# Kernel tuning notes

Hardware: AMD Instinct MI355X
Metric: run time of the kernel (lower is better)

The kernel has to match this reference:

```python
import jax, jax.numpy as jnp
import numpy as np


def _ens_linear(x, W, b):
    # x: [B,T,Din], W: [E,Din,Dout], b: [E,Dout] -> [E,B,T,Dout]
    return jnp.einsum('btd,edh->ebth', x, W) + b[:, None, None, :]


def _gilr_scan(v, f):
    # h_t = f_t * h_{t-1} + (1 - f_t) * v_t, h_0 = 0 (tie-input-gate linear recurrence)
    def comb(c1, c2):
        a1, b1 = c1
        a2, b2 = c2
        return a2 * a1, a2 * b1 + b2
    _, h = jax.lax.associative_scan(comb, (f, (1.0 - f) * v), axis=1)
    return h


def setup_inputs() -> dict:
    key = jax.random.key(0)
    ks = jax.random.split(key, 7)
    B, T, Din, D = 8, 4096, 512, 512
    x = jax.random.normal(ks[0], (B, T, Din), dtype=jnp.float32)
    s_in = 1.0 / np.sqrt(Din)
    s = 1.0 / np.sqrt(D)
    W_in = jax.random.uniform(ks[1], (2, Din, D), jnp.float32, -s_in, s_in)
    b_in = jax.random.uniform(ks[2], (2, D), jnp.float32, -s_in, s_in)
    W_mid = jax.random.uniform(ks[3], (4, D, D), jnp.float32, -s, s)
    b_mid = jax.random.uniform(ks[4], (4, D), jnp.float32, -s, s)
    W_out = jax.random.uniform(ks[5], (D, D), jnp.float32, -s, s)
    b_out = jax.random.uniform(ks[6], (D,), jnp.float32, -s, s)
    return {"x": x, "W_in": W_in, "b_in": b_in, "W_mid": W_mid,
            "b_mid": b_mid, "W_out": W_out, "b_out": b_out}


def reference(x, W_in, b_in, W_mid, b_mid, W_out, b_out):
    # in_proj (ensemble of 2): u[0] -> v, u[1] -> f
    u = _ens_linear(x, W_in, b_in)
    v = jnp.tanh(u[0])
    f = jax.nn.sigmoid(u[1])
    # first gated linear recurrence (hidden_pre starts at zeros)
    v = _gilr_scan(v, f)
    hidden_pre = v[:, -1:, :]
    # middle_proj (ensemble of 4): f, i, o, z
    u = _ens_linear(v, W_mid, b_mid)
    f2 = jax.nn.sigmoid(u[0])
    i = jax.nn.sigmoid(u[1])
    o = jax.nn.sigmoid(u[2])
    z = jnp.tanh(u[3])
    # second gated linear recurrence (hidden_middle starts at zeros)
    out = _gilr_scan(i * z, f2)
    hidden_middle = out[:, -1:, :]
    out = out * o
    out = out @ W_out + b_out
    hidden = jnp.concatenate((hidden_pre, hidden_middle), axis=-1)
    hidden = jnp.transpose(hidden, (1, 0, 2))  # [1, B, 2D]
    return out, hidden
```

## Files before the change

### kernel.cpp

```cpp
#include <hip/hip_runtime.h>

typedef short short8 __attribute__((ext_vector_type(8)));
typedef float float4v __attribute__((ext_vector_type(4)));
typedef unsigned short u16;
typedef unsigned int u32;

#define T_LEN 4096
#define DDIM 512
#define BATCH 8
#define MROWS 32768
#define CH 32
#define NC 128

__device__ __forceinline__ u16 f2b(float x) {
    unsigned u = __float_as_uint(x);
    unsigned r = (u + 0x7FFFu + ((u >> 16) & 1u)) >> 16;
    return (u16)r;
}
__device__ __forceinline__ float b2f(u16 h) {
    return __uint_as_float((u32)h << 16);
}
__device__ __forceinline__ float sigm(float x) {
    return __builtin_amdgcn_rcpf(1.f + __builtin_amdgcn_exp2f(-1.44269504f * x));
}
__device__ __forceinline__ float tanh_fast(float x) {
    return 1.f - 2.f * __builtin_amdgcn_rcpf(1.f + __builtin_amdgcn_exp2f(2.88539008f * x));
}

__device__ __forceinline__ void gl2lds16(const u16* g, u16* l) {
    __builtin_amdgcn_global_load_lds(
        (const __attribute__((address_space(1))) void*)g,
        (__attribute__((address_space(3))) void*)l, 16, 0, 0);
}

__global__ __launch_bounds__(256) void cvt_x(const float* __restrict__ x,
                                             u16* __restrict__ xb, size_t n) {
    size_t i = ((size_t)blockIdx.x * 256 + threadIdx.x) * 4;
    if (i < n) {
        float4v v = *(const float4v*)&x[i];
        ushort4 p;
        p.x = f2b(v[0]); p.y = f2b(v[1]); p.z = f2b(v[2]); p.w = f2b(v[3]);
        *(ushort4*)&xb[i] = p;
    }
}

__global__ __launch_bounds__(256) void cvt_wt(const float* __restrict__ W,
                                              u16* __restrict__ Wt, int N) {
    int idx = blockIdx.x * 256 + threadIdx.x;
    if (idx >= N * 512) return;
    int j = idx >> 9;
    int k = idx & 511;
    int e = j >> 9, h = j & 511;
    Wt[(size_t)j * 512 + k] = f2b(W[((size_t)e * 512 + k) * 512 + h]);
}

template <int MODE>
__global__ __launch_bounds__(512, 4) void gemm_act(
    const u16* __restrict__ A, const u16* __restrict__ Bt,
    const float* __restrict__ bias, void* __restrict__ o0v,
    void* __restrict__ o1v, void* __restrict__ o2v, void* __restrict__ o3v) {
    constexpr int K = 512;
    constexpr int BK = 32;
    constexpr int NKT = K / BK;
    constexpr int LBA = 256 * 32;
    constexpr int LBB = 128 * 32;
    constexpr int GX = (MODE == 1) ? 8 : (MODE == 2) ? 16 : 4;
    constexpr int NWG = 128 * GX;
    __shared__ u16 lsA[3][LBA];
    __shared__ u16 lsB[3][LBB];
    const int tid = threadIdx.x;
    const int lane = tid & 63;
    const int wid = tid >> 6;
    const int wr = wid >> 1;
    const int wc = wid & 1;
    const int l0 = lane & 15, lh = lane >> 4;

    const int h = blockIdx.x;
    const int l = (h & 7) * (NWG / 8) + (h >> 3);
    const int bn0 = (l & (GX - 1)) * 128;
    const int bm0 = (l / GX) * 256;

    float4v acc[4][4];
#pragma unroll
    for (int m = 0; m < 4; ++m)
#pragma unroll
        for (int n = 0; n < 4; ++n) acc[m][n] = (float4v){0.f, 0.f, 0.f, 0.f};

    int growA[2], gchA[2], growB, gchB;
#pragma unroll
    for (int i = 0; i < 2; ++i) {
        int flat = i * 512 + tid;
        growA[i] = flat >> 2;
        gchA[i] = (((flat & 3) ^ ((growA[i] >> 1) & 3))) * 8;
    }
    growB = tid >> 2;
    gchB = (((tid & 3) ^ ((growB >> 1) & 3))) * 8;

#define STAGE(buf, kt)                                                        \
    {                                                                         \
        const int k0 = (kt) * BK;                                             \
        _Pragma("unroll") for (int i = 0; i < 2; ++i)                         \
            gl2lds16(&A[(size_t)(bm0 + growA[i]) * K + k0 + gchA[i]],         \
                     &lsA[buf][(i * 512 + tid) * 8]);                         \
        gl2lds16(&Bt[(size_t)(bn0 + growB) * K + k0 + gchB],                  \
                 &lsB[buf][tid * 8]);                                         \
    }

    STAGE(0, 0);
    STAGE(1, 1);

    for (int kt = 0; kt < NKT; ++kt) {
        const int cur = kt % 3;
        if (kt + 1 < NKT)
            asm volatile("s_waitcnt vmcnt(3)" ::: "memory");
        else
            asm volatile("s_waitcnt vmcnt(0)" ::: "memory");
        __builtin_amdgcn_s_barrier();
        __builtin_amdgcn_sched_barrier(0);
        if (kt + 2 < NKT) STAGE((kt + 2) % 3, kt + 2);
        short8 af[4], bf[4];
#pragma unroll
        for (int m = 0; m < 4; ++m) {
            int r = wr * 64 + m * 16 + l0;
            af[m] = *(const short8*)&lsA[cur][r * 32 + ((lh ^ ((r >> 1) & 3)) * 8)];
        }
#pragma unroll
        for (int n = 0; n < 4; ++n) {
            int r = wc * 64 + n * 16 + l0;
            bf[n] = *(const short8*)&lsB[cur][r * 32 + ((lh ^ ((r >> 1) & 3)) * 8)];
        }
        asm volatile("s_waitcnt lgkmcnt(0)" ::: "memory");
        __builtin_amdgcn_sched_barrier(0);
        __builtin_amdgcn_s_setprio(1);
#pragma unroll
        for (int m = 0; m < 4; ++m)
#pragma unroll
            for (int n = 0; n < 4; ++n)
                acc[m][n] = __builtin_amdgcn_mfma_f32_16x16x32_bf16(
                    af[m], bf[n], acc[m][n], 0, 0, 0);
        __builtin_amdgcn_s_setprio(0);
    }
#undef STAGE

#pragma unroll
    for (int m = 0; m < 4; ++m) {
#pragma unroll
        for (int n = 0; n < 4; ++n) {
            int col = bn0 + wc * 64 + n * 16 + l0;
            float bv = bias[col];
#pragma unroll
            for (int r = 0; r < 4; ++r) {
                int rw = bm0 + wr * 64 + m * 16 + lh * 4 + r;
                float u = acc[m][n][r] + bv;
                size_t oidx = (size_t)rw * 512 + (col & 511);
                if (MODE == 1) {
                    if (col < 512)
                        ((u16*)o0v)[oidx] = f2b(tanh_fast(u));
                    else
                        ((u16*)o1v)[oidx] = f2b(sigm(u));
                } else if (MODE == 2) {
                    int e = col >> 9;
                    if (e == 0)
                        ((u16*)o0v)[oidx] = f2b(sigm(u));
                    else if (e == 1)
                        ((u16*)o1v)[oidx] = f2b(sigm(u));
                    else if (e == 2)
                        ((u16*)o2v)[oidx] = f2b(sigm(u));
                    else
                        ((u16*)o3v)[oidx] = f2b(tanh_fast(u));
                } else {
                    ((float*)o0v)[oidx] = u;
                }
            }
        }
    }
}

template <int S>
__global__ __launch_bounds__(128) void scan_p1(const u16* __restrict__ f,
                                               const u16* __restrict__ v,
                                               const u16* __restrict__ z,
                                               float* __restrict__ cA,
                                               float* __restrict__ cB) {
    int d0 = threadIdx.x * 4;
    int c = blockIdx.x & (NC - 1);
    int b = blockIdx.x >> 7;
    size_t base = ((size_t)b * T_LEN + c * CH) * DDIM + d0;
    float Aa[4] = {1.f, 1.f, 1.f, 1.f}, Bb[4] = {0.f, 0.f, 0.f, 0.f};
    for (int t = 0; t < CH; ++t) {
        ushort4 fq = *(const ushort4*)&f[base];
        ushort4 vq = *(const ushort4*)&v[base];
        float ff[4] = {b2f(fq.x), b2f(fq.y), b2f(fq.z), b2f(fq.w)};
        float gg[4] = {b2f(vq.x), b2f(vq.y), b2f(vq.z), b2f(vq.w)};
        if (S == 2) {
            ushort4 zq = *(const ushort4*)&z[base];
            gg[0] *= b2f(zq.x); gg[1] *= b2f(zq.y);
            gg[2] *= b2f(zq.z); gg[3] *= b2f(zq.w);
        }
#pragma unroll
        for (int j = 0; j < 4; ++j) {
            float g = (1.f - ff[j]) * gg[j];
            Bb[j] = ff[j] * Bb[j] + g;
            Aa[j] *= ff[j];
        }
        base += DDIM;
    }
    size_t ci = (size_t)c * 4096 + b * DDIM + d0;
#pragma unroll
    for (int j = 0; j < 4; ++j) {
        cA[ci + j] = Aa[j];
        cB[ci + j] = Bb[j];
    }
}

__global__ __launch_bounds__(256) void scan_p2(float* __restrict__ cA,
                                               const float* __restrict__ cB) {
    int ln = blockIdx.x * 256 + threadIdx.x;
    float h = 0.f;
    for (int c = 0; c < NC; ++c) {
        size_t ix = (size_t)c * 4096 + ln;
        float a = cA[ix], bb = cB[ix];
        cA[ix] = h;
        h = a * h + bb;
    }
}

template <int S>
__global__ __launch_bounds__(128) void scan_p3(
    const u16* __restrict__ f, const u16* __restrict__ v,
    const u16* __restrict__ z, const u16* __restrict__ o,
    const float* __restrict__ cA, u16* __restrict__ hb,
    float* __restrict__ hid) {
    int d0 = threadIdx.x * 4;
    int c = blockIdx.x & (NC - 1);
    int b = blockIdx.x >> 7;
    size_t base = ((size_t)b * T_LEN + c * CH) * DDIM + d0;
    size_t ci = (size_t)c * 4096 + b * DDIM + d0;
    float h[4] = {cA[ci], cA[ci + 1], cA[ci + 2], cA[ci + 3]};
    for (int t = 0; t < CH; ++t) {
        ushort4 fq = *(const ushort4*)&f[base];
        ushort4 vq = *(const ushort4*)&v[base];
        float ff[4] = {b2f(fq.x), b2f(fq.y), b2f(fq.z), b2f(fq.w)};
        float gg[4] = {b2f(vq.x), b2f(vq.y), b2f(vq.z), b2f(vq.w)};
        if (S == 2) {
            ushort4 zq = *(const ushort4*)&z[base];
            gg[0] *= b2f(zq.x); gg[1] *= b2f(zq.y);
            gg[2] *= b2f(zq.z); gg[3] *= b2f(zq.w);
        }
        float w[4];
#pragma unroll
        for (int j = 0; j < 4; ++j) {
            float g = (1.f - ff[j]) * gg[j];
            h[j] = ff[j] * h[j] + g;
            w[j] = h[j];
        }
        if (S == 2) {
            ushort4 oq = *(const ushort4*)&o[base];
            w[0] *= b2f(oq.x); w[1] *= b2f(oq.y);
            w[2] *= b2f(oq.z); w[3] *= b2f(oq.w);
        }
        ushort4 p;
        p.x = f2b(w[0]); p.y = f2b(w[1]); p.z = f2b(w[2]); p.w = f2b(w[3]);
        *(ushort4*)&hb[base] = p;
        base += DDIM;
    }
    if (c == NC - 1) {
#pragma unroll
        for (int j = 0; j < 4; ++j)
            hid[b * 1024 + (S == 1 ? 0 : 512) + d0 + j] = h[j];
    }
}

extern "C" void kernel_launch(void* const* d_in, const int* in_sizes, int n_in,
                              void* d_out, int out_size, void* d_ws,
                              size_t ws_size, hipStream_t stream) {
    const float* x = (const float*)d_in[0];
    const float* W_in = (const float*)d_in[1];
    const float* b_in = (const float*)d_in[2];
    const float* W_mid = (const float*)d_in[3];
    const float* b_mid = (const float*)d_in[4];
    const float* W_out = (const float*)d_in[5];
    const float* b_out = (const float*)d_in[6];
    float* out = (float*)d_out;
    char* ws = (char*)d_ws;

    const size_t MB = 1u << 20;
    const size_t MD = (size_t)MROWS * DDIM;

    u16* wt_in = (u16*)(ws);
    u16* wt_mid = (u16*)(ws + 1 * MB);
    u16* wt_out = (u16*)(ws + 3 * MB);
    u16* hb = (u16*)(ws + 4 * MB);
    u16* S0 = (u16*)(ws + 36 * MB);
    u16* S1 = (u16*)(ws + 68 * MB);
    u16* S2 = (u16*)(ws + 100 * MB);
    u16* S3 = (u16*)(ws + 132 * MB);
    float* cA = (float*)(ws + 164 * MB);
    float* cB = (float*)(ws + 166 * MB);
    float* hid = out + MD;

    cvt_x<<<(int)(MD / 4 / 256), 256, 0, stream>>>(x, hb, MD);
    cvt_wt<<<(1024 * 512) / 256, 256, 0, stream>>>(W_in, wt_in, 1024);
    cvt_wt<<<(2048 * 512) / 256, 256, 0, stream>>>(W_mid, wt_mid, 2048);
    cvt_wt<<<(512 * 512) / 256, 256, 0, stream>>>(W_out, wt_out, 512);

    gemm_act<1><<<1024, 512, 0, stream>>>(hb, wt_in, b_in, S0, S1, nullptr,
                                          nullptr);
    scan_p1<1><<<1024, 128, 0, stream>>>(S1, S0, nullptr, cA, cB);
    scan_p2<<<16, 256, 0, stream>>>(cA, cB);
    scan_p3<1><<<1024, 128, 0, stream>>>(S1, S0, nullptr, nullptr, cA, hb, hid);

    gemm_act<2><<<2048, 512, 0, stream>>>(hb, wt_mid, b_mid, S0, S1, S2, S3);
    scan_p1<2><<<1024, 128, 0, stream>>>(S0, S1, S3, cA, cB);
    scan_p2<<<16, 256, 0, stream>>>(cA, cB);
    scan_p3<2><<<1024, 128, 0, stream>>>(S0, S1, S3, S2, cA, hb, hid);

    gemm_act<3><<<512, 512, 0, stream>>>(hb, wt_out, b_out, out, nullptr,
                                         nullptr, nullptr);
}
```

Baseline: 292.7 us.

## Interleave gate weight columns so GEMM epilogue precomputes gated scan input

Weight columns are reordered during conversion so each wave's accumulator tile holds the matching f/v (or f/i/o/z) gates for the same hidden index. The GEMM epilogue then computes (1-f)*tanh(v) and (1-f)*i*z directly and writes only f, g and o. The scan kernels read two streams instead of three or four. This removes one bf16 intermediate buffer per stage and its write/read traffic, at the cost of a more complex epilogue with strided column writes of 16-element groups.

New measurement: 259.7 us. 11.3% less time.

```diff
diff --git a/kernel.cpp b/kernel.cpp
--- a/kernel.cpp
+++ b/kernel.cpp
@@ -44,21 +44,25 @@
     }
 }
 
+template <int MODE>
 __global__ __launch_bounds__(256) void cvt_wt(const float* __restrict__ W,
                                               u16* __restrict__ Wt, int N) {
     int idx = blockIdx.x * 256 + threadIdx.x;
     if (idx >= N * 512) return;
     int j = idx >> 9;
     int k = idx & 511;
-    int e = j >> 9, h = j & 511;
-    Wt[(size_t)j * 512 + k] = f2b(W[((size_t)e * 512 + k) * 512 + h]);
+    int gate, d;
+    if (MODE == 1) { gate = (j >> 4) & 1; d = (j >> 5) * 16 + (j & 15); }
+    else if (MODE == 2) { gate = (j >> 4) & 3; d = (j >> 6) * 16 + (j & 15); }
+    else { gate = 0; d = j; }
+    Wt[(size_t)j * 512 + k] = f2b(W[((size_t)gate * 512 + k) * 512 + d]);
 }
 
 template <int MODE>
 __global__ __launch_bounds__(512, 4) void gemm_act(
     const u16* __restrict__ A, const u16* __restrict__ Bt,
     const float* __restrict__ bias, void* __restrict__ o0v,
-    void* __restrict__ o1v, void* __restrict__ o2v, void* __restrict__ o3v) {
+    void* __restrict__ o1v, void* __restrict__ o2v) {
     constexpr int K = 512;
     constexpr int BK = 32;
     constexpr int NKT = K / BK;
@@ -142,44 +146,64 @@
     }
 #undef STAGE
 
-#pragma unroll
-    for (int m = 0; m < 4; ++m) {
-#pragma unroll
-        for (int n = 0; n < 4; ++n) {
-            int col = bn0 + wc * 64 + n * 16 + l0;
-            float bv = bias[col];
+    if (MODE == 3) {
+#pragma unroll
+        for (int m = 0; m < 4; ++m) {
+#pragma unroll
+            for (int n = 0; n < 4; ++n) {
+                int col = bn0 + wc * 64 + n * 16 + l0;
+                float bv = bias[col];
+#pragma unroll
+                for (int r = 0; r < 4; ++r) {
+                    int rw = bm0 + wr * 64 + m * 16 + lh * 4 + r;
+                    ((float*)o0v)[(size_t)rw * 512 + col] = acc[m][n][r] + bv;
+                }
+            }
+        }
+    } else if (MODE == 1) {
+        const int base5 = (bn0 + wc * 64) >> 5;
+#pragma unroll
+        for (int p = 0; p < 2; ++p) {
+            const int d = (base5 + p) * 16 + l0;
+            const float bvv = bias[d], bvf = bias[512 + d];
+#pragma unroll
+            for (int m = 0; m < 4; ++m) {
+#pragma unroll
+                for (int r = 0; r < 4; ++r) {
+                    int rw = bm0 + wr * 64 + m * 16 + lh * 4 + r;
+                    float f1 = sigm(acc[m][2 * p + 1][r] + bvf);
+                    float g = (1.f - f1) * tanh_fast(acc[m][2 * p][r] + bvv);
+                    size_t oidx = (size_t)rw * 512 + d;
+                    ((u16*)o0v)[oidx] = f2b(f1);
+                    ((u16*)o1v)[oidx] = f2b(g);
+                }
+            }
+        }
+    } else {
+        const int d = ((bn0 + wc * 64) >> 6) * 16 + l0;
+        const float bv0 = bias[d], bv1 = bias[512 + d];
+        const float bv2 = bias[1024 + d], bv3 = bias[1536 + d];
+#pragma unroll
+        for (int m = 0; m < 4; ++m) {
 #pragma unroll
             for (int r = 0; r < 4; ++r) {
                 int rw = bm0 + wr * 64 + m * 16 + lh * 4 + r;
-                float u = acc[m][n][r] + bv;
-                size_t oidx = (size_t)rw * 512 + (col & 511);
-                if (MODE == 1) {
-                    if (col < 512)
-                        ((u16*)o0v)[oidx] = f2b(tanh_fast(u));
-                    else
-                        ((u16*)o1v)[oidx] = f2b(sigm(u));
-                } else if (MODE == 2) {
-                    int e = col >> 9;
-                    if (e == 0)
-                        ((u16*)o0v)[oidx] = f2b(sigm(u));
-                    else if (e == 1)
-                        ((u16*)o1v)[oidx] = f2b(sigm(u));
-                    else if (e == 2)
-                        ((u16*)o2v)[oidx] = f2b(sigm(u));
-                    else
-                        ((u16*)o3v)[oidx] = f2b(tanh_fast(u));
-                } else {
-                    ((float*)o0v)[oidx] = u;
-                }
+                float f2 = sigm(acc[m][0][r] + bv0);
+                float ii = sigm(acc[m][1][r] + bv1);
+                float oo = sigm(acc[m][2][r] + bv2);
+                float zz = tanh_fast(acc[m][3][r] + bv3);
+                float g = (1.f - f2) * ii * zz;
+                size_t oidx = (size_t)rw * 512 + d;
+                ((u16*)o0v)[oidx] = f2b(f2);
+                ((u16*)o1v)[oidx] = f2b(g);
+                ((u16*)o2v)[oidx] = f2b(oo);
             }
         }
     }
 }
 
-template <int S>
 __global__ __launch_bounds__(128) void scan_p1(const u16* __restrict__ f,
-                                               const u16* __restrict__ v,
-                                               const u16* __restrict__ z,
+                                               const u16* __restrict__ g,
                                                float* __restrict__ cA,
                                                float* __restrict__ cB) {
     int d0 = threadIdx.x * 4;
@@ -189,18 +213,12 @@
     float Aa[4] = {1.f, 1.f, 1.f, 1.f}, Bb[4] = {0.f, 0.f, 0.f, 0.f};
     for (int t = 0; t < CH; ++t) {
         ushort4 fq = *(const ushort4*)&f[base];
-        ushort4 vq = *(const ushort4*)&v[base];
+        ushort4 gq = *(const ushort4*)&g[base];
         float ff[4] = {b2f(fq.x), b2f(fq.y), b2f(fq.z), b2f(fq.w)};
-        float gg[4] = {b2f(vq.x), b2f(vq.y), b2f(vq.z), b2f(vq.w)};
-        if (S == 2) {
-            ushort4 zq = *(const ushort4*)&z[base];
-            gg[0] *= b2f(zq.x); gg[1] *= b2f(zq.y);
-            gg[2] *= b2f(zq.z); gg[3] *= b2f(zq.w);
-        }
+        float gg[4] = {b2f(gq.x), b2f(gq.y), b2f(gq.z), b2f(gq.w)};
 #pragma unroll
         for (int j = 0; j < 4; ++j) {
-            float g = (1.f - ff[j]) * gg[j];
-            Bb[j] = ff[j] * Bb[j] + g;
+            Bb[j] = ff[j] * Bb[j] + gg[j];
             Aa[j] *= ff[j];
         }
         base += DDIM;
@@ -227,10 +245,9 @@
 
 template <int S>
 __global__ __launch_bounds__(128) void scan_p3(
-    const u16* __restrict__ f, const u16* __restrict__ v,
-    const u16* __restrict__ z, const u16* __restrict__ o,
-    const float* __restrict__ cA, u16* __restrict__ hb,
-    float* __restrict__ hid) {
+    const u16* __restrict__ f, const u16* __restrict__ g,
+    const u16* __restrict__ o, const float* __restrict__ cA,
+    u16* __restrict__ hb, float* __restrict__ hid) {
     int d0 = threadIdx.x * 4;
     int c = blockIdx.x & (NC - 1);
     int b = blockIdx.x >> 7;
@@ -239,19 +256,13 @@
     float h[4] = {cA[ci], cA[ci + 1], cA[ci + 2], cA[ci + 3]};
     for (int t = 0; t < CH; ++t) {
         ushort4 fq = *(const ushort4*)&f[base];
-        ushort4 vq = *(const ushort4*)&v[base];
+        ushort4 gq = *(const ushort4*)&g[base];
         float ff[4] = {b2f(fq.x), b2f(fq.y), b2f(fq.z), b2f(fq.w)};
-        float gg[4] = {b2f(vq.x), b2f(vq.y), b2f(vq.z), b2f(vq.w)};
-        if (S == 2) {
-            ushort4 zq = *(const ushort4*)&z[base];
-            gg[0] *= b2f(zq.x); gg[1] *= b2f(zq.y);
-            gg[2] *= b2f(zq.z); gg[3] *= b2f(zq.w);
-        }
+        float gg[4] = {b2f(gq.x), b2f(gq.y), b2f(gq.z), b2f(gq.w)};
         float w[4];
 #pragma unroll
         for (int j = 0; j < 4; ++j) {
-            float g = (1.f - ff[j]) * gg[j];
-            h[j] = ff[j] * h[j] + g;
+            h[j] = ff[j] * h[j] + gg[j];
             w[j] = h[j];
         }
         if (S == 2) {
@@ -294,27 +305,25 @@
     u16* S0 = (u16*)(ws + 36 * MB);
     u16* S1 = (u16*)(ws + 68 * MB);
     u16* S2 = (u16*)(ws + 100 * MB);
-    u16* S3 = (u16*)(ws + 132 * MB);
     float* cA = (float*)(ws + 164 * MB);
     float* cB = (float*)(ws + 166 * MB);
     float* hid = out + MD;
 
     cvt_x<<<(int)(MD / 4 / 256), 256, 0, stream>>>(x, hb, MD);
-    cvt_wt<<<(1024 * 512) / 256, 256, 0, stream>>>(W_in, wt_in, 1024);
-    cvt_wt<<<(2048 * 512) / 256, 256, 0, stream>>>(W_mid, wt_mid, 2048);
-    cvt_wt<<<(512 * 512) / 256, 256, 0, stream>>>(W_out, wt_out, 512);
-
-    gemm_act<1><<<1024, 512, 0, stream>>>(hb, wt_in, b_in, S0, S1, nullptr,
-                                          nullptr);
-    scan_p1<1><<<1024, 128, 0, stream>>>(S1, S0, nullptr, cA, cB);
+    cvt_wt<1><<<(1024 * 512) / 256, 256, 0, stream>>>(W_in, wt_in, 1024);
+    cvt_wt<2><<<(2048 * 512) / 256, 256, 0, stream>>>(W_mid, wt_mid, 2048);
+    cvt_wt<3><<<(512 * 512) / 256, 256, 0, stream>>>(W_out, wt_out, 512);
+
+    gemm_act<1><<<1024, 512, 0, stream>>>(hb, wt_in, b_in, S0, S1, nullptr);
+    scan_p1<<<1024, 128, 0, stream>>>(S0, S1, cA, cB);
     scan_p2<<<16, 256, 0, stream>>>(cA, cB);
-    scan_p3<1><<<1024, 128, 0, stream>>>(S1, S0, nullptr, nullptr, cA, hb, hid);
-
-    gemm_act<2><<<2048, 512, 0, stream>>>(hb, wt_mid, b_mid, S0, S1, S2, S3);
-    scan_p1<2><<<1024, 128, 0, stream>>>(S0, S1, S3, cA, cB);
+    scan_p3<1><<<1024, 128, 0, stream>>>(S0, S1, nullptr, cA, hb, hid);
+
+    gemm_act<2><<<2048, 512, 0, stream>>>(hb, wt_mid, b_mid, S0, S1, S2);
+    scan_p1<<<1024, 128, 0, stream>>>(S0, S1, cA, cB);
     scan_p2<<<16, 256, 0, stream>>>(cA, cB);
-    scan_p3<2><<<1024, 128, 0, stream>>>(S0, S1, S3, S2, cA, hb, hid);
+    scan_p3<2><<<1024, 128, 0, stream>>>(S0, S1, S2, cA, hb, hid);
 
     gemm_act<3><<<512, 512, 0, stream>>>(hb, wt_out, b_out, out, nullptr,
-                                         nullptr, nullptr);
-}
+                                         nullptr);
+}
```
